# Optimization experiments

Hardware: AMD Instinct MI355X
Metric: run time of the kernel (lower is better)

Reference implementation:

```python
import jax, jax.numpy as jnp
import numpy as np

FEATURE_SCALE = 0.25  # cfg.feature_scale
G = 4                 # deformable/offset groups
K = 3                 # deform kernel size
KK = K * K
PAD = 1


def conv2d(x, w, b=None):
    y = jax.lax.conv_general_dilated(x, w, (1, 1), ((PAD, PAD), (PAD, PAD)),
                                     dimension_numbers=('NCHW', 'OIHW', 'NCHW'))
    return y if b is None else y + b[None, :, None, None]


def bilinear_upsample_ac(x, fs):
    # F.interpolate(mode='bilinear', align_corners=True, scale_factor=fs)
    b, c, H, W = x.shape
    Ho, Wo = H * fs, W * fs
    sy = jnp.arange(Ho, dtype=x.dtype) * ((H - 1) / (Ho - 1))
    sx = jnp.arange(Wo, dtype=x.dtype) * ((W - 1) / (Wo - 1))
    y0 = jnp.clip(jnp.floor(sy).astype(jnp.int32), 0, H - 2)
    x0 = jnp.clip(jnp.floor(sx).astype(jnp.int32), 0, W - 2)
    wy = (sy - y0)[None, None, :, None]
    wx = (sx - x0)[None, None, None, :]
    rows = x[:, :, y0, :] * (1 - wy) + x[:, :, y0 + 1, :] * wy
    return rows[:, :, :, x0] * (1 - wx) + rows[:, :, :, x0 + 1] * wx


def deform_conv(x, offset, mask, w):
    # torchvision.ops.deform_conv2d, stride 1, pad 1, weight groups = 1,
    # offset/mask groups = G. offset layout: (b, G*KK*2, H, W), (dy, dx) pairs.
    b, C, H, W = x.shape
    Cg = C // G
    off = offset.reshape(b, G, KK, 2, H, W)
    ii = (jnp.arange(KK) // K).reshape(1, 1, KK, 1, 1).astype(x.dtype)
    jj = (jnp.arange(KK) % K).reshape(1, 1, KK, 1, 1).astype(x.dtype)
    ys = jnp.arange(H, dtype=x.dtype).reshape(1, 1, 1, H, 1)
    xs = jnp.arange(W, dtype=x.dtype).reshape(1, 1, 1, 1, W)
    py = ys - PAD + ii + off[:, :, :, 0]   # (b,G,KK,H,W)
    px = xs - PAD + jj + off[:, :, :, 1]
    xt = x.reshape(b, G, Cg, H, W).transpose(0, 1, 3, 4, 2)  # (b,G,H,W,Cg)
    y0f = jnp.floor(py)
    x0f = jnp.floor(px)
    wy = py - y0f
    wx = px - x0f
    y0 = y0f.astype(jnp.int32)
    x0 = x0f.astype(jnp.int32)
    bi = jnp.arange(b).reshape(b, 1, 1, 1, 1)
    gi = jnp.arange(G).reshape(1, G, 1, 1, 1)

    def corner(yi, xi, wgt):
        valid = ((yi >= 0) & (yi < H) & (xi >= 0) & (xi < W)).astype(x.dtype)
        v = xt[bi, gi, jnp.clip(yi, 0, H - 1), jnp.clip(xi, 0, W - 1)]  # (b,G,KK,H,W,Cg)
        return v * (wgt * valid)[..., None]

    s = (corner(y0, x0, (1 - wy) * (1 - wx)) + corner(y0, x0 + 1, (1 - wy) * wx)
         + corner(y0 + 1, x0, wy * (1 - wx)) + corner(y0 + 1, x0 + 1, wy * wx))
    s = s * mask.reshape(b, G, KK, H, W)[..., None]
    wr = w.reshape(w.shape[0], G, Cg, KK)
    return jnp.einsum('bgkhwc,ogck->bohw', s, wr)


def _align(sou_list, ref_list, params):
    cat_feat, offset_vs = [], []
    for i in (3, 2, 1):
        sou, ref = sou_list[i - 1], ref_list[i - 1]
        b, C, H, W = sou.shape
        Cg = C // G
        off_w, off_b, mod_w, mod_b, reg_w = params[i]
        off_in = jnp.concatenate([sou.reshape(b, G, Cg, H, W),
                                  ref.reshape(b, G, Cg, H, W)], axis=2)
        off_in = off_in.reshape(b * G, 2 * Cg, H, W)
        offset = conv2d(off_in, off_w, off_b).reshape(b, G * 2 * KK, H, W)
        rng = min(H, W) * 0.5 / 2
        offset_map = rng * 2 * jax.nn.sigmoid(offset) - rng
        modulator = 2.0 * jax.nn.sigmoid(conv2d(sou, mod_w, mod_b))
        feat = deform_conv(sou, offset_map, modulator, reg_w)
        fs = int(1 // (FEATURE_SCALE / 2 ** (i - 1)))
        oy = jnp.mean(offset_map[:, 0::2], axis=1, keepdims=True)
        ox = jnp.mean(offset_map[:, 1::2], axis=1, keepdims=True)
        ov = bilinear_upsample_ac(jnp.concatenate([oy, ox], axis=1), fs) * fs
        cat_feat.append(feat)
        offset_vs.append(ov)
    return tuple(cat_feat) + tuple(offset_vs)


def setup_inputs() -> dict:
    key = jax.random.key(0)
    ks = jax.random.split(key, 32)
    d = {}
    shapes = {1: (2, 64, 128, 128), 2: (2, 64, 64, 64), 3: (2, 64, 32, 32)}
    k = 0
    for i in (1, 2, 3):
        d[f'sou{i}'] = jax.random.normal(ks[k], shapes[i], jnp.float32); k += 1
        d[f'ref{i}'] = jax.random.normal(ks[k], shapes[i], jnp.float32); k += 1
    Cg = 64 // G
    for i in (1, 2, 3):
        d[f'off_w{i}'] = jax.random.normal(ks[k], (2 * KK, 2 * Cg, K, K), jnp.float32) * 0.05; k += 1
        d[f'off_b{i}'] = jax.random.normal(ks[k], (2 * KK,), jnp.float32) * 0.05; k += 1
        d[f'mod_w{i}'] = jax.random.normal(ks[k], (G * KK, 64, K, K), jnp.float32) * 0.05; k += 1
        d[f'mod_b{i}'] = jax.random.normal(ks[k], (G * KK,), jnp.float32) * 0.05; k += 1
        d[f'reg_w{i}'] = jax.random.normal(ks[k], (64, 64, K, K), jnp.float32) * 0.05; k += 1
    return d


def reference(sou1, sou2, sou3, ref1, ref2, ref3,
              off_w1, off_b1, mod_w1, mod_b1, reg_w1,
              off_w2, off_b2, mod_w2, mod_b2, reg_w2,
              off_w3, off_b3, mod_w3, mod_b3, reg_w3):
    params = {1: (off_w1, off_b1, mod_w1, mod_b1, reg_w1),
              2: (off_w2, off_b2, mod_w2, mod_b2, reg_w2),
              3: (off_w3, off_b3, mod_w3, mod_b3, reg_w3)}
    return _align([sou1, sou2, sou3], [ref1, ref2, ref3], params)
```

## Files before the change

kernel.cpp:

```cpp
#include <hip/hip_runtime.h>

typedef __attribute__((ext_vector_type(8))) short short8;
typedef __attribute__((ext_vector_type(4))) float f32x4;

__device__ __forceinline__ float sigmoidf_(float x) { return 1.f / (1.f + __expf(-x)); }
__device__ __forceinline__ unsigned bf16rne(float x) {
    unsigned b = __float_as_uint(x);
    return (b + 0x7FFFu + ((b >> 16) & 1u)) >> 16;
}


struct P {
    const float *sou0, *sou1, *sou2;
    const float *ref0, *ref1, *ref2;
    const float *ob0, *ob1, *ob2;
    const float *mb0, *mb1, *mb2;
    float* out;
    float* ws;
};

union U {
    uint4 u4; int4 i4; short8 s8; f32x4 f4;
};

__global__ __launch_bounds__(256) void repack_all(
    const float* __restrict__ ow0, const float* __restrict__ mw0, const float* __restrict__ rw0,
    const float* __restrict__ ow1, const float* __restrict__ mw1, const float* __restrict__ rw1,
    const float* __restrict__ ow2, const float* __restrict__ mw2, const float* __restrict__ rw2,
    float* __restrict__ dst) {
    const int lvl = blockIdx.y;
    const float* ow = lvl == 0 ? ow0 : (lvl == 1 ? ow1 : ow2);
    const float* mw = lvl == 0 ? mw0 : (lvl == 1 ? mw1 : mw2);
    const float* rw = lvl == 0 ? rw0 : (lvl == 1 ? rw1 : rw2);
    unsigned* d = (unsigned*)(dst + lvl * 62784);
    int i = blockIdx.x * 256 + threadIdx.x;
    if (i < 18432) {
        int jw = i & 3;
        int lane = (i >> 2) & 63;
        int t3 = i >> 8;
        int ks = t3 % 18, wvu = t3 / 18;
        int o = wvu * 16 + (lane & 15);
        int c0 = ks * 32 + (lane >> 4) * 8 + 2 * jw;
        int g0 = c0 / 144, r0 = c0 % 144;
        int c1 = c0 + 1;
        int g1 = c1 / 144, r1 = c1 % 144;
        float w0 = rw[o * 576 + (g0 * 16 + (r0 & 15)) * 9 + (r0 >> 4)];
        float w1 = rw[o * 576 + (g1 * 16 + (r1 & 15)) * 9 + (r1 >> 4)];
        d[i] = bf16rne(w0) | (bf16rne(w1) << 16);
    } else if (i < 23552) {
        int o2 = i - 18432;
        int jw = o2 & 3;
        int lane = (o2 >> 2) & 63;
        int t2 = o2 >> 8;
        int nt = t2 & 1;
        int hk = t2 >> 1;
        int ks = hk % 5, h = hk / 5;
        int n = nt * 16 + (lane & 15);
        int K = ks * 32 + (lane >> 4) * 8 + 2 * jw;
        int tap = K >> 4, ch = K & 15;
        bool ok = (n < 18) && (tap < 9);
        float w0 = ok ? ow[n * 288 + (h * 16 + ch) * 9 + tap] : 0.f;
        float w1 = ok ? ow[n * 288 + (h * 16 + ch + 1) * 9 + tap] : 0.f;
        d[36864 + o2] = bf16rne(w0) | (bf16rne(w1) << 16);
    } else if (i < 37376) {
        int o3 = i - 23552;
        int jw = o3 & 3;
        int lane = (o3 >> 2) & 63;
        int t3 = o3 >> 8;
        int nt = t3 % 3, tc = t3 / 3;
        int tap = tc >> 1, c = tc & 1;
        int n = nt * 16 + (lane & 15);
        int ic0 = c * 32 + (lane >> 4) * 8 + 2 * jw;
        float w0 = (n < 36) ? mw[n * 576 + ic0 * 9 + tap] : 0.f;
        float w1 = (n < 36) ? mw[n * 576 + (ic0 + 1) * 9 + tap] : 0.f;
        d[41984 + o3] = bf16rne(w0) | (bf16rne(w1) << 16);
    }
}

__global__ __launch_bounds__(256) void k1_prep(P p) {
    __shared__ __align__(16) char smem[28512];
    const int t = blockIdx.x;
    float* ws = p.ws;
    const int tid = threadIdx.x;

    int lvl, j;
    if (t < 512) { lvl = 0; j = t; }
    else if (t < 640) { lvl = 1; j = t - 512; }
    else { lvl = 2; j = t - 640; }
    const int logW = 7 - lvl;
    const int W = 1 << logW, H = W, HW = H * W;
    const int nper = 256 >> (2 * lvl);
    const int qb = j % nper, b = j / nper;
    const int q0 = qb * 64;
    const int hlo = q0 >> logW;
    const int xlo = q0 & (W - 1);
    const int cols = (W >= 64) ? 66 : 34;
    const int rcTot = (W >= 64) ? 198 : 136;
    const float* sou = lvl == 0 ? p.sou0 : (lvl == 1 ? p.sou1 : p.sou2);
    const float* ref = lvl == 0 ? p.ref0 : (lvl == 1 ? p.ref1 : p.ref2);
    const float* base_s = sou + (size_t)b * 64 * HW;
    const float* base_r = ref + (size_t)b * 64 * HW;
    unsigned* ldsW = (unsigned*)smem;
    const bool sact = tid < rcTot;
    const int srow = tid / cols, scol = tid - srow * cols;
    const int grow = hlo - 1 + srow, gcol = xlo - 1 + scol;
    const bool inb = sact && grow >= 0 && grow < H && gcol >= 0 && gcol < W;
    const size_t goff = inb ? ((size_t)grow * W + gcol) : 0;

#pragma unroll
    for (int c8 = 0; c8 < 8; ++c8) {
        const float* p0 = base_s + (size_t)(c8 * 8) * HW;
        float v[8];
#pragma unroll
        for (int jj = 0; jj < 8; ++jj) v[jj] = inb ? p0[(size_t)jj * HW + goff] : 0.f;
        if (sact) {
            uint4 wv;
            wv.x = bf16rne(v[0]) | (bf16rne(v[1]) << 16);
            wv.y = bf16rne(v[2]) | (bf16rne(v[3]) << 16);
            wv.z = bf16rne(v[4]) | (bf16rne(v[5]) << 16);
            wv.w = bf16rne(v[6]) | (bf16rne(v[7]) << 16);
            *(uint4*)&ldsW[tid * 36 + c8 * 4] = wv;
        }
    }
    __syncthreads();

    unsigned* XTb = (unsigned*)(ws + 4919232) +
                    (lvl == 0 ? 0 : (lvl == 1 ? 1048576 : 1310720));
#pragma unroll
    for (int u = 0; u < 2; ++u) {
        const int idx = tid * 2 + u;
        const int px = idx >> 3, gh = idx & 7;
        const int g = gh >> 1, half = gh & 1;
        const int rc = ((px >> logW) + 1) * cols + (px & (W - 1)) + 1;
        uint4 v = *(const uint4*)&ldsW[rc * 36 + g * 8 + half * 4];
        *(uint4*)(XTb + ((size_t)(b * 4 + g) * HW + q0 + px) * 8 + half * 4) = v;
    }

    const int wvu = __builtin_amdgcn_readfirstlane(tid >> 6);
    const int lane = tid & 63, quad = lane >> 4, lo16 = lane & 15;
    const int qg = q0 + wvu * 16 + lo16;
    const int rowB = (qg >> logW) - hlo;
    const int colB = (qg & (W - 1)) - xlo;
    const unsigned short* ldsS = (const unsigned short*)smem;
    const unsigned* WREPu = (const unsigned*)(ws + 4730880 + lvl * 62784);
    const unsigned* WBO2 = WREPu + 36864;
    const unsigned* WBM = WREPu + 41984;

    f32x4 accM[3], accO[4][2];
#pragma unroll
    for (int nt = 0; nt < 3; ++nt) accM[nt] = (f32x4){0.f, 0.f, 0.f, 0.f};
#pragma unroll
    for (int g = 0; g < 4; ++g)
#pragma unroll
        for (int nt = 0; nt < 2; ++nt) accO[g][nt] = (f32x4){0.f, 0.f, 0.f, 0.f};

#pragma unroll
    for (int tap = 0; tap < 9; ++tap) {
        const int ky = tap / 3, kx = tap - ky * 3;
        const int rc = (rowB + ky) * cols + colB + kx;
#pragma unroll
        for (int c = 0; c < 2; ++c) {
            U au; au.s8 = *(const short8*)&ldsS[rc * 72 + c * 32 + quad * 8];
#pragma unroll
            for (int nt = 0; nt < 3; ++nt) {
                U bu;
                bu.u4 = *(const uint4*)(WBM + (((tap * 2 + c) * 3 + nt) * 64 + lane) * 4);
                accM[nt] = __builtin_amdgcn_mfma_f32_16x16x32_bf16(au.s8, bu.s8, accM[nt], 0, 0, 0);
            }
        }
    }
#pragma unroll
    for (int ks = 0; ks < 5; ++ks) {
        const int Kbase = ks * 32 + quad * 8;
        const int tap = min(Kbase >> 4, 8);
        const int ky = tap / 3, kx = tap - ky * 3;
        const int rc = (rowB + ky) * cols + colB + kx;
        const int choff = Kbase & 15;
#pragma unroll
        for (int g = 0; g < 4; ++g) {
            U au; au.s8 = *(const short8*)&ldsS[rc * 72 + g * 16 + choff];
#pragma unroll
            for (int nt = 0; nt < 2; ++nt) {
                U bu;
                bu.u4 = *(const uint4*)(WBO2 + ((ks * 2 + nt) * 64 + lane) * 4);
                accO[g][nt] =
                    __builtin_amdgcn_mfma_f32_16x16x32_bf16(au.s8, bu.s8, accO[g][nt], 0, 0, 0);
            }
        }
    }
    __syncthreads();

#pragma unroll
    for (int c8 = 0; c8 < 8; ++c8) {
        const float* p0 = base_r + (size_t)(c8 * 8) * HW;
        float v[8];
#pragma unroll
        for (int jj = 0; jj < 8; ++jj) v[jj] = inb ? p0[(size_t)jj * HW + goff] : 0.f;
        if (sact) {
            uint4 wv;
            wv.x = bf16rne(v[0]) | (bf16rne(v[1]) << 16);
            wv.y = bf16rne(v[2]) | (bf16rne(v[3]) << 16);
            wv.z = bf16rne(v[4]) | (bf16rne(v[5]) << 16);
            wv.w = bf16rne(v[6]) | (bf16rne(v[7]) << 16);
            *(uint4*)&ldsW[tid * 36 + c8 * 4] = wv;
        }
    }
    __syncthreads();

#pragma unroll
    for (int ks = 0; ks < 5; ++ks) {
        const int Kbase = ks * 32 + quad * 8;
        const int tap = min(Kbase >> 4, 8);
        const int ky = tap / 3, kx = tap - ky * 3;
        const int rc = (rowB + ky) * cols + colB + kx;
        const int choff = Kbase & 15;
#pragma unroll
        for (int g = 0; g < 4; ++g) {
            U au; au.s8 = *(const short8*)&ldsS[rc * 72 + g * 16 + choff];
#pragma unroll
            for (int nt = 0; nt < 2; ++nt) {
                U bu;
                bu.u4 = *(const uint4*)(WBO2 + (((5 + ks) * 2 + nt) * 64 + lane) * 4);
                accO[g][nt] =
                    __builtin_amdgcn_mfma_f32_16x16x32_bf16(au.s8, bu.s8, accO[g][nt], 0, 0, 0);
            }
        }
    }

    {
        const float* bias = lvl == 0 ? p.mb0 : (lvl == 1 ? p.mb1 : p.mb2);
        float* MOD = ws + (lvl == 0 ? 3096576 : (lvl == 1 ? 4276224 : 4571136));
#pragma unroll
        for (int nt = 0; nt < 3; ++nt) {
            const int o = nt * 16 + lo16;
            if (o < 36) {
                const float bb = bias[o];
                float* op = MOD + (size_t)(b * 36 + o) * HW + q0 + wvu * 16 + quad * 4;
                *(float4*)op = make_float4(2.f * sigmoidf_(accM[nt][0] + bb),
                                           2.f * sigmoidf_(accM[nt][1] + bb),
                                           2.f * sigmoidf_(accM[nt][2] + bb),
                                           2.f * sigmoidf_(accM[nt][3] + bb));
            }
        }
    }
    {
        const float* bias = lvl == 0 ? p.ob0 : (lvl == 1 ? p.ob1 : p.ob2);
        float* OFFM = ws + (lvl == 0 ? 0 : (lvl == 1 ? 2359296 : 2949120));
        const float rng = 0.25f * (float)H;
        float macc[4] = {0.f, 0.f, 0.f, 0.f};
#pragma unroll
        for (int g = 0; g < 4; ++g)
#pragma unroll
            for (int nt = 0; nt < 2; ++nt) {
                const int o = nt * 16 + lo16;
                if (o < 18) {
                    const float bb = bias[o];
                    float ovv[4];
#pragma unroll
                    for (int rg = 0; rg < 4; ++rg)
                        ovv[rg] = rng * (2.f * sigmoidf_(accO[g][nt][rg] + bb) - 1.f);
                    float* op = OFFM + (size_t)(b * 72 + g * 18 + o) * HW + q0 + wvu * 16 + quad * 4;
                    *(float4*)op = make_float4(ovv[0], ovv[1], ovv[2], ovv[3]);
#pragma unroll
                    for (int rg = 0; rg < 4; ++rg) macc[rg] += ovv[rg];
                }
            }
        const bool odd = (lo16 & 1) != 0;
        float my[4], mx[4];
#pragma unroll
        for (int rg = 0; rg < 4; ++rg) {
            my[rg] = odd ? 0.f : macc[rg];
            mx[rg] = odd ? macc[rg] : 0.f;
        }
#pragma unroll
        for (int m = 1; m < 16; m <<= 1) {
#pragma unroll
            for (int rg = 0; rg < 4; ++rg) {
                my[rg] += __shfl_xor(my[rg], m);
                mx[rg] += __shfl_xor(mx[rg], m);
            }
        }
        if (lo16 == 0) {
            float* MEAN = ws + (lvl == 0 ? 4644864 : (lvl == 1 ? 4710400 : 4726784));
            const int pxb = q0 + wvu * 16 + quad * 4;
            const float inv = 1.f / 36.f;
            *(float4*)(MEAN + (size_t)(b * 2) * HW + pxb) =
                make_float4(my[0] * inv, my[1] * inv, my[2] * inv, my[3] * inv);
            *(float4*)(MEAN + (size_t)(b * 2 + 1) * HW + pxb) =
                make_float4(mx[0] * inv, mx[1] * inv, mx[2] * inv, mx[3] * inv);
        }
    }
}

__global__ __launch_bounds__(256) void k2_fused(P p) {
    __shared__ __align__(16) unsigned lds[32 * 100];
    const int t = blockIdx.x;
    float* ws = p.ws;
    const int tid = threadIdx.x;
    if (t < 1344) {
        int lvl, j;
        if (t < 1024) { lvl = 0; j = t; }
        else if (t < 1280) { lvl = 1; j = t - 1024; }
        else { lvl = 2; j = t - 1280; }
        const int logW = 7 - lvl;
        const int W = 1 << logW, H = W, HW = H * W;
        const int nper = 512 >> (2 * lvl);
        const int qb = j % nper, b = j / nper;
        const int q0 = qb * 32;
        const float* OFFM = ws + (lvl == 0 ? 0 : (lvl == 1 ? 2359296 : 2949120));
        const float* MOD = ws + (lvl == 0 ? 3096576 : (lvl == 1 ? 4276224 : 4571136));
        const unsigned* XTb = (const unsigned*)(ws + 4919232) +
                              (lvl == 0 ? 0 : (lvl == 1 ? 1048576 : 1310720));
        const unsigned* WB = (const unsigned*)(ws + 4730880 + lvl * 62784);
        float* outp = p.out + (lvl == 0 ? 655360 : (lvl == 1 ? 131072 : 0));
        const int wvu = __builtin_amdgcn_readfirstlane(tid >> 6);
        const int lane = tid & 63, quad = lane >> 4, lo16 = lane & 15;
        f32x4 acc[2];
        acc[0] = (f32x4){0.f, 0.f, 0.f, 0.f};
        acc[1] = (f32x4){0.f, 0.f, 0.f, 0.f};
        for (int c = 0; c < 3; ++c) {
            if (c) __syncthreads();
#pragma unroll
            for (int it = 0; it < 2; ++it) {
                const int task = it * 256 + tid;
                if (task < 384) {
                    const int gkl = task >> 5, px = task & 31;
                    const int gk = c * 12 + gkl;
                    const int g = gk / 9, k = gk - g * 9;
                    const int q = q0 + px;
                    const int h = q >> logW, xp = q & (W - 1);
                    const int ky = k / 3, kx = k - ky * 3;
                    float dy = OFFM[(size_t)(b * 72 + g * 18 + 2 * k) * HW + q];
                    float dx = OFFM[(size_t)(b * 72 + g * 18 + 2 * k + 1) * HW + q];
                    float m = MOD[(size_t)(b * 36 + g * 9 + k) * HW + q];
                    float py = (float)(h - 1 + ky) + dy;
                    float pxx = (float)(xp - 1 + kx) + dx;
                    float y0f = floorf(py), x0f = floorf(pxx);
                    float wy = py - y0f, wx = pxx - x0f;
                    int y0 = (int)y0f, x0 = (int)x0f;
                    const unsigned* xg = XTb + (size_t)(b * 4 + g) * HW * 8;
                    float s[16];
#pragma unroll
                    for (int cc = 0; cc < 16; ++cc) s[cc] = 0.f;
#pragma unroll
                    for (int cor = 0; cor < 4; ++cor) {
                        int yy = y0 + (cor >> 1), xx = x0 + (cor & 1);
                        float cw = ((cor >> 1) ? wy : 1.f - wy) * ((cor & 1) ? wx : 1.f - wx);
                        cw = (yy >= 0 && yy < H && xx >= 0 && xx < W) ? cw * m : 0.f;
                        int yc = min(max(yy, 0), H - 1), xc = min(max(xx, 0), W - 1);
                        const uint4* cp = (const uint4*)(xg + (size_t)((yc << logW) + xc) * 8);
                        unsigned cbuf[8];
                        *(uint4*)&cbuf[0] = cp[0];
                        *(uint4*)&cbuf[4] = cp[1];
#pragma unroll
                        for (int pr = 0; pr < 8; ++pr) {
                            float lo = __uint_as_float(cbuf[pr] << 16);
                            float hi = __uint_as_float(cbuf[pr] & 0xFFFF0000u);
                            s[2 * pr] = fmaf(cw, lo, s[2 * pr]);
                            s[2 * pr + 1] = fmaf(cw, hi, s[2 * pr + 1]);
                        }
                    }
                    unsigned* dp = &lds[px * 100 + gkl * 8];
                    uint4 w0, w1;
                    w0.x = bf16rne(s[0]) | (bf16rne(s[1]) << 16);
                    w0.y = bf16rne(s[2]) | (bf16rne(s[3]) << 16);
                    w0.z = bf16rne(s[4]) | (bf16rne(s[5]) << 16);
                    w0.w = bf16rne(s[6]) | (bf16rne(s[7]) << 16);
                    w1.x = bf16rne(s[8]) | (bf16rne(s[9]) << 16);
                    w1.y = bf16rne(s[10]) | (bf16rne(s[11]) << 16);
                    w1.z = bf16rne(s[12]) | (bf16rne(s[13]) << 16);
                    w1.w = bf16rne(s[14]) | (bf16rne(s[15]) << 16);
                    *(uint4*)dp = w0;
                    *(uint4*)(dp + 4) = w1;
                }
            }
            __syncthreads();
            uint4 bfr[6];
#pragma unroll
            for (int k6 = 0; k6 < 6; ++k6)
                bfr[k6] = *(const uint4*)(WB + (((wvu * 18 + c * 6 + k6) * 64 + lane) << 2));
#pragma unroll
            for (int k6 = 0; k6 < 6; ++k6) {
                U bu; bu.u4 = bfr[k6];
#pragma unroll
                for (int mt = 0; mt < 2; ++mt) {
                    const int px = mt * 16 + lo16;
                    U au;
                    au.u4 = *(const uint4*)&lds[px * 100 + k6 * 16 + quad * 4];
                    acc[mt] = __builtin_amdgcn_mfma_f32_16x16x32_bf16(au.s8, bu.s8, acc[mt], 0, 0, 0);
                }
            }
        }
        float* op = outp + (size_t)(b * 64 + wvu * 16 + lo16) * HW + q0;
#pragma unroll
        for (int mt = 0; mt < 2; ++mt)
#pragma unroll
            for (int rg = 0; rg < 4; ++rg)
                op[mt * 16 + quad * 4 + rg] = acc[mt][rg];
    } else {
        int flat = ((t - 1344) * 256 + tid) * 4;
        int lvl = flat >> 20;
        int r = flat & 1048575;
        int b = r >> 19, c = (r >> 18) & 1;
        int pix = r & 262143;
        int yo = pix >> 9, xo = pix & 511;
        const int H = 128 >> lvl, W = H;
        const float* MEAN = ws + (lvl == 0 ? 4644864 : (lvl == 1 ? 4710400 : 4726784));
        const float* m = MEAN + (size_t)(b * 2 + c) * H * W;
        float* o = p.out + (lvl == 0 ? 4849664 : (lvl == 1 ? 3801088 : 2752512)) +
                   ((size_t)(b * 2 + c) * 512 + yo) * 512 + xo;
        const float fs = (float)(4 << lvl);
        const float sc = (float)(H - 1) * (1.f / 511.f);
        float sy = yo * sc;
        int y0 = min((int)sy, H - 2);
        float wy = sy - (float)y0;
        float rr[4];
#pragma unroll
        for (int u = 0; u < 4; ++u) {
            float sx = (float)(xo + u) * sc;
            int x0 = min((int)sx, W - 2);
            float wx = sx - (float)x0;
            float v00 = m[y0 * W + x0], v01 = m[y0 * W + x0 + 1];
            float v10 = m[(y0 + 1) * W + x0], v11 = m[(y0 + 1) * W + x0 + 1];
            float r0 = v00 * (1.f - wy) + v10 * wy;
            float r1 = v01 * (1.f - wy) + v11 * wy;
            rr[u] = (r0 * (1.f - wx) + r1 * wx) * fs;
        }
        *(float4*)o = make_float4(rr[0], rr[1], rr[2], rr[3]);
    }
}

extern "C" void kernel_launch(void* const* d_in, const int* in_sizes, int n_in,
                              void* d_out, int out_size, void* d_ws, size_t ws_size,
                              hipStream_t stream) {
    const float* fin[21];
    for (int i = 0; i < 21; ++i) fin[i] = (const float*)d_in[i];
    P p;
    if (in_sizes[1] == in_sizes[0]) {
        p.sou0 = fin[0]; p.ref0 = fin[1];
        p.sou1 = fin[2]; p.ref1 = fin[3];
        p.sou2 = fin[4]; p.ref2 = fin[5];
    } else {
        p.sou0 = fin[0]; p.sou1 = fin[1]; p.sou2 = fin[2];
        p.ref0 = fin[3]; p.ref1 = fin[4]; p.ref2 = fin[5];
    }
    p.ob0 = fin[7]; p.mb0 = fin[9];
    p.ob1 = fin[12]; p.mb1 = fin[14];
    p.ob2 = fin[17]; p.mb2 = fin[19];
    p.out = (float*)d_out;
    p.ws = (float*)d_ws;

    repack_all<<<dim3(146, 3), 256, 0, stream>>>(
        fin[6], fin[8], fin[10], fin[11], fin[13], fin[15], fin[16], fin[18], fin[20],
        p.ws + 4730880);
    k1_prep<<<dim3(672), 256, 0, stream>>>(p);
    k2_fused<<<dim3(4416), 256, 0, stream>>>(p);
}
```

Measured before the change: 175.7 us.

## Batch global loads into 32-register groups, hoist B-fragments, remap k2 block order

The staging loop that loads sou/ref channels now issues 32 global loads per batch (two halves) before converting and writing to LDS, giving more loads in flight. The B-operand weight fragments for the offset MFMA loops are hoisted out of the group loop so they load once per k-step. In k2_fused, block indices are permuted so adjacent pairs of tiles land on blocks spaced eight apart, likely to spread neighbouring tiles across XCDs for cache locality. The larger register array raises VGPR pressure and may reduce occupancy.

```diff
diff --git a/kernel.cpp b/kernel.cpp
--- a/kernel.cpp
+++ b/kernel.cpp
@@ -107,19 +107,26 @@
     const bool inb = sact && grow >= 0 && grow < H && gcol >= 0 && gcol < W;
     const size_t goff = inb ? ((size_t)grow * W + gcol) : 0;
 
-#pragma unroll
-    for (int c8 = 0; c8 < 8; ++c8) {
-        const float* p0 = base_s + (size_t)(c8 * 8) * HW;
-        float v[8];
-#pragma unroll
-        for (int jj = 0; jj < 8; ++jj) v[jj] = inb ? p0[(size_t)jj * HW + goff] : 0.f;
+    float v[32];
+#pragma unroll
+    for (int hb = 0; hb < 2; ++hb) {
+#pragma unroll
+        for (int c8 = 0; c8 < 4; ++c8) {
+            const float* p0 = base_s + (size_t)((hb * 4 + c8) * 8) * HW;
+#pragma unroll
+            for (int jj = 0; jj < 8; ++jj)
+                v[c8 * 8 + jj] = inb ? p0[(size_t)jj * HW + goff] : 0.f;
+        }
         if (sact) {
-            uint4 wv;
-            wv.x = bf16rne(v[0]) | (bf16rne(v[1]) << 16);
-            wv.y = bf16rne(v[2]) | (bf16rne(v[3]) << 16);
-            wv.z = bf16rne(v[4]) | (bf16rne(v[5]) << 16);
-            wv.w = bf16rne(v[6]) | (bf16rne(v[7]) << 16);
-            *(uint4*)&ldsW[tid * 36 + c8 * 4] = wv;
+#pragma unroll
+            for (int c8 = 0; c8 < 4; ++c8) {
+                uint4 wv;
+                wv.x = bf16rne(v[c8 * 8 + 0]) | (bf16rne(v[c8 * 8 + 1]) << 16);
+                wv.y = bf16rne(v[c8 * 8 + 2]) | (bf16rne(v[c8 * 8 + 3]) << 16);
+                wv.z = bf16rne(v[c8 * 8 + 4]) | (bf16rne(v[c8 * 8 + 5]) << 16);
+                wv.w = bf16rne(v[c8 * 8 + 6]) | (bf16rne(v[c8 * 8 + 7]) << 16);
+                *(uint4*)&ldsW[tid * 36 + (hb * 4 + c8) * 4] = wv;
+            }
         }
     }
     __syncthreads();
@@ -132,8 +139,8 @@
         const int px = idx >> 3, gh = idx & 7;
         const int g = gh >> 1, half = gh & 1;
         const int rc = ((px >> logW) + 1) * cols + (px & (W - 1)) + 1;
-        uint4 v = *(const uint4*)&ldsW[rc * 36 + g * 8 + half * 4];
-        *(uint4*)(XTb + ((size_t)(b * 4 + g) * HW + q0 + px) * 8 + half * 4) = v;
+        uint4 vv = *(const uint4*)&ldsW[rc * 36 + g * 8 + half * 4];
+        *(uint4*)(XTb + ((size_t)(b * 4 + g) * HW + q0 + px) * 8 + half * 4) = vv;
     }
 
     const int wvu = __builtin_amdgcn_readfirstlane(tid >> 6);
@@ -176,34 +183,39 @@
         const int ky = tap / 3, kx = tap - ky * 3;
         const int rc = (rowB + ky) * cols + colB + kx;
         const int choff = Kbase & 15;
+        U bu0, bu1;
+        bu0.u4 = *(const uint4*)(WBO2 + ((ks * 2 + 0) * 64 + lane) * 4);
+        bu1.u4 = *(const uint4*)(WBO2 + ((ks * 2 + 1) * 64 + lane) * 4);
 #pragma unroll
         for (int g = 0; g < 4; ++g) {
             U au; au.s8 = *(const short8*)&ldsS[rc * 72 + g * 16 + choff];
-#pragma unroll
-            for (int nt = 0; nt < 2; ++nt) {
-                U bu;
-                bu.u4 = *(const uint4*)(WBO2 + ((ks * 2 + nt) * 64 + lane) * 4);
-                accO[g][nt] =
-                    __builtin_amdgcn_mfma_f32_16x16x32_bf16(au.s8, bu.s8, accO[g][nt], 0, 0, 0);
-            }
+            accO[g][0] = __builtin_amdgcn_mfma_f32_16x16x32_bf16(au.s8, bu0.s8, accO[g][0], 0, 0, 0);
+            accO[g][1] = __builtin_amdgcn_mfma_f32_16x16x32_bf16(au.s8, bu1.s8, accO[g][1], 0, 0, 0);
         }
     }
     __syncthreads();
 
 #pragma unroll
-    for (int c8 = 0; c8 < 8; ++c8) {
-        const float* p0 = base_r + (size_t)(c8 * 8) * HW;
-        float v[8];
-#pragma unroll
-        for (int jj = 0; jj < 8; ++jj) v[jj] = inb ? p0[(size_t)jj * HW + goff] : 0.f;
+    for (int hb = 0; hb < 2; ++hb) {
+#pragma unroll
+        for (int c8 = 0; c8 < 4; ++c8) {
+            const float* p0 = base_r + (size_t)((hb * 4 + c8) * 8) * HW;
+#pragma unroll
+            for (int jj = 0; jj < 8; ++jj)
+                v[c8 * 8 + jj] = inb ? p0[(size_t)jj * HW + goff] : 0.f;
+        }
         if (sact) {
-            uint4 wv;
-            wv.x = bf16rne(v[0]) | (bf16rne(v[1]) << 16);
-            wv.y = bf16rne(v[2]) | (bf16rne(v[3]) << 16);
-            wv.z = bf16rne(v[4]) | (bf16rne(v[5]) << 16);
-            wv.w = bf16rne(v[6]) | (bf16rne(v[7]) << 16);
-            *(uint4*)&ldsW[tid * 36 + c8 * 4] = wv;
-        }
+#pragma unroll
+            for (int c8 = 0; c8 < 4; ++c8) {
+                uint4 wv;
+                wv.x = bf16rne(v[c8 * 8 + 0]) | (bf16rne(v[c8 * 8 + 1]) << 16);
+                wv.y = bf16rne(v[c8 * 8 + 2]) | (bf16rne(v[c8 * 8 + 3]) << 16);
+                wv.z = bf16rne(v[c8 * 8 + 4]) | (bf16rne(v[c8 * 8 + 5]) << 16);
+                wv.w = bf16rne(v[c8 * 8 + 6]) | (bf16rne(v[c8 * 8 + 7]) << 16);
+                *(uint4*)&ldsW[tid * 36 + (hb * 4 + c8) * 4] = wv;
+            }
+        }
+        if (hb == 0) __syncthreads();
     }
     __syncthreads();
 
@@ -214,16 +226,14 @@
         const int ky = tap / 3, kx = tap - ky * 3;
         const int rc = (rowB + ky) * cols + colB + kx;
         const int choff = Kbase & 15;
+        U bu0, bu1;
+        bu0.u4 = *(const uint4*)(WBO2 + (((5 + ks) * 2 + 0) * 64 + lane) * 4);
+        bu1.u4 = *(const uint4*)(WBO2 + (((5 + ks) * 2 + 1) * 64 + lane) * 4);
 #pragma unroll
         for (int g = 0; g < 4; ++g) {
             U au; au.s8 = *(const short8*)&ldsS[rc * 72 + g * 16 + choff];
-#pragma unroll
-            for (int nt = 0; nt < 2; ++nt) {
-                U bu;
-                bu.u4 = *(const uint4*)(WBO2 + (((5 + ks) * 2 + nt) * 64 + lane) * 4);
-                accO[g][nt] =
-                    __builtin_amdgcn_mfma_f32_16x16x32_bf16(au.s8, bu.s8, accO[g][nt], 0, 0, 0);
-            }
+            accO[g][0] = __builtin_amdgcn_mfma_f32_16x16x32_bf16(au.s8, bu0.s8, accO[g][0], 0, 0, 0);
+            accO[g][1] = __builtin_amdgcn_mfma_f32_16x16x32_bf16(au.s8, bu1.s8, accO[g][1], 0, 0, 0);
         }
     }
 
@@ -298,10 +308,12 @@
     float* ws = p.ws;
     const int tid = threadIdx.x;
     if (t < 1344) {
-        int lvl, j;
-        if (t < 1024) { lvl = 0; j = t; }
-        else if (t < 1280) { lvl = 1; j = t - 1024; }
-        else { lvl = 2; j = t - 1280; }
+        const int x = t & 7, r = t >> 3;
+        int lvl, u;
+        if (r < 128) { lvl = 0; u = x + ((r >> 1) << 3); }
+        else if (r < 160) { lvl = 1; u = x + (((r - 128) >> 1) << 3); }
+        else { lvl = 2; u = x + (((r - 160) >> 1) << 3); }
+        const int j = 2 * u + (r & 1);
         const int logW = 7 - lvl;
         const int W = 1 << logW, H = W, HW = H * W;
         const int nper = 512 >> (2 * lvl);
```

After: 176.7 us. No clear change (+0.6%).
